# Optimization experiments

Measured on AMD Instinct MI355X. Metric: run time of the kernel, lower is better.

The kernel has to match this reference:

```python
import jax, jax.numpy as jnp
import numpy as np
from functools import partial

H = 512          # hidden_size
H4 = H // 4      # goal hidden size
ENC = 8          # enc_steps
DEC = 12         # dec_steps
PRED = 2         # pred_dim (ETH)
B = 512          # batch


def _lin(k, i, o, s=0.05):
    kw, kb = jax.random.split(k)
    return jax.random.normal(kw, (i, o), jnp.float32) * s, jax.random.normal(kb, (o,), jnp.float32) * s


def setup_inputs() -> dict:
    key = jax.random.key(0)
    ks = jax.random.split(key, 32)
    d = {"inputs": jax.random.normal(ks[0], (B, ENC, 6), jnp.float32)}
    d["embed_w"], d["embed_b"] = _lin(ks[1], 6, H)
    d["reg_w"], d["reg_b"] = _lin(ks[2], H, PRED)
    d["ea_w"], d["ea_b"] = _lin(ks[3], H4, 1)
    d["da_w"], d["da_b"] = _lin(ks[4], H4, 1)
    d["e2g_w"], d["e2g_b"] = _lin(ks[5], H, H4)
    d["e2d_w"], d["e2d_b"] = _lin(ks[6], H, H)
    d["gh2i_w"], d["gh2i_b"] = _lin(ks[7], H4, H4)
    d["dh2i_w"], d["dh2i_b"] = _lin(ks[8], H, H)
    d["gh2t_w"], d["gh2t_b"] = _lin(ks[9], H4, H)
    d["g2e_w"], d["g2e_b"] = _lin(ks[10], H4, H4)
    d["g2d_w"], d["g2d_b"] = _lin(ks[11], H4, H4)
    d["enc_wih"], _ = _lin(ks[12], H + H4, 3 * H)
    d["enc_whh"], _ = _lin(ks[13], H, 3 * H)
    d["enc_bih"] = jax.random.normal(ks[14], (3 * H,), jnp.float32) * 0.05
    d["enc_bhh"] = jax.random.normal(ks[15], (3 * H,), jnp.float32) * 0.05
    d["goal_wih"], _ = _lin(ks[16], H4, 3 * H4)
    d["goal_whh"], _ = _lin(ks[17], H4, 3 * H4)
    d["goal_bih"] = jax.random.normal(ks[18], (3 * H4,), jnp.float32) * 0.05
    d["goal_bhh"] = jax.random.normal(ks[19], (3 * H4,), jnp.float32) * 0.05
    d["dec_wih"], _ = _lin(ks[20], H + H4, 3 * H)
    d["dec_whh"], _ = _lin(ks[21], H, 3 * H)
    d["dec_bih"] = jax.random.normal(ks[22], (3 * H,), jnp.float32) * 0.05
    d["dec_bhh"] = jax.random.normal(ks[23], (3 * H,), jnp.float32) * 0.05
    return d


def _gru(x, h, wih, whh, bih, bhh):
    gi = x @ wih + bih          # [B, 3H]
    gh = h @ whh + bhh
    ir, iz, inn = jnp.split(gi, 3, axis=-1)
    hr, hz, hn = jnp.split(gh, 3, axis=-1)
    r = jax.nn.sigmoid(ir + hr)
    z = jax.nn.sigmoid(iz + hz)
    n = jnp.tanh(inn + r * hn)
    return (1.0 - z) * n + z * h


def reference(inputs, embed_w, embed_b, reg_w, reg_b, ea_w, ea_b, da_w, da_b,
              e2g_w, e2g_b, e2d_w, e2d_b, gh2i_w, gh2i_b, dh2i_w, dh2i_b,
              gh2t_w, gh2t_b, g2e_w, g2e_b, g2d_w, g2d_b,
              enc_wih, enc_whh, enc_bih, enc_bhh,
              goal_wih, goal_whh, goal_bih, goal_bhh,
              dec_wih, dec_whh, dec_bih, dec_bhh):
    relu = jax.nn.relu
    b = inputs.shape[0]
    traj_input = relu(inputs @ embed_w + embed_b)           # [B, ENC, H]

    def sge(goal_hidden):
        def gstep(carry, _):
            gh, gi = carry
            gh = _gru(gi, gh, goal_wih, goal_whh, goal_bih, goal_bhh)
            gi = relu(gh @ gh2i_w + gh2i_b)
            return (gh, gi), gh
        gi0 = jnp.zeros((b, H4), traj_input.dtype)
        _, goals = jax.lax.scan(gstep, (goal_hidden, gi0), None, length=DEC)  # [DEC,B,H4]
        goal_traj = relu(goals @ gh2t_w + gh2t_b) @ reg_w + reg_b             # [DEC,B,PRED]
        goal_for_dec = relu(goals @ g2d_w + g2d_b)                            # [DEC,B,H4]
        gfe = relu(goals @ g2e_w + g2e_b).transpose(1, 0, 2)                  # [B,DEC,H4]
        logits = relu(jnp.tanh(gfe) @ ea_w + ea_b)[..., 0]                    # [B,DEC]
        attn = jax.nn.softmax(logits, axis=1)
        goal_for_enc = jnp.einsum('bt,bth->bh', attn, gfe)
        return goal_for_dec, goal_for_enc, goal_traj.transpose(1, 0, 2)

    def decoder(dec_hidden, gfd):
        gfd_b = gfd.transpose(1, 0, 2)  # [B,DEC,H4]
        steps = jnp.arange(DEC)
        def dstep(dh, t):
            mask = (steps >= t)[None, :, None]
            gdi = jnp.where(mask, gfd_b, 0.0)                      # zeros before t, faithful to torch
            logits = relu(jnp.tanh(gdi) @ da_w + da_b)[..., 0]     # [B,DEC]
            attn = jax.nn.softmax(logits, axis=1)
            ctx = jnp.einsum('bt,bth->bh', attn, gdi)
            ddi = relu(dh @ dh2i_w + dh2i_b)
            x = jnp.concatenate([ctx, ddi], axis=-1)
            dh = _gru(x, dh, dec_wih, dec_whh, dec_bih, dec_bhh)
            return dh, dh @ reg_w + reg_b
        _, traj = jax.lax.scan(dstep, dec_hidden, steps)           # [DEC,B,PRED]
        return traj.transpose(1, 0, 2)

    def estep(carry, x_t):
        teh, gfe = carry
        teh = _gru(jnp.concatenate([x_t, gfe], axis=1), teh,
                   enc_wih, enc_whh, enc_bih, enc_bhh)
        goal_hidden = relu(teh @ e2g_w + e2g_b)
        dec_hidden = relu(teh @ e2d_w + e2d_b)
        gfd, gfe, goal_traj = sge(goal_hidden)
        dec_traj = decoder(dec_hidden, gfd)
        return (teh, gfe), (goal_traj, dec_traj)

    teh0 = jnp.zeros((b, H), traj_input.dtype)
    gfe0 = jnp.zeros((b, H4), traj_input.dtype)
    _, (all_goal, all_dec) = jax.lax.scan(estep, (teh0, gfe0),
                                          traj_input.transpose(1, 0, 2))
    # [ENC,B,DEC,PRED] -> [B,ENC,DEC,PRED]
    return all_goal.transpose(1, 0, 2, 3), all_dec.transpose(1, 0, 2, 3)
```

## Files before the change

kernel.cpp:

```cpp
#include <hip/hip_runtime.h>


typedef unsigned short u16;
typedef __attribute__((ext_vector_type(8))) short bf16x8;
typedef __attribute__((ext_vector_type(4))) float f32x4;

static __device__ __forceinline__ float b2f(u16 u) {
  union { float f; unsigned int i; } x; x.i = ((unsigned int)u) << 16; return x.f;
}
static __device__ __forceinline__ u16 f2b(float f) {
  unsigned int u = __float_as_uint(f);
  unsigned int r = (u + 0x7FFFu + ((u >> 16) & 1u)) >> 16;
  return (u16)r;
}
static __device__ __forceinline__ float fsig(float x) {
  return __fdividef(1.f, 1.f + __expf(-x));
}
static __device__ __forceinline__ float ftanh(float x) {
  return 1.f - __fdividef(2.f, __expf(2.f * x) + 1.f);
}

__global__ __launch_bounds__(256) void transpose_f2b(const float* __restrict__ in,
                                                     u16* __restrict__ out,
                                                     int K, int N) {
  __shared__ u16 t[32][33];
  int n0 = blockIdx.x * 32, k0 = blockIdx.y * 32;
  int x = threadIdx.x & 31, y = threadIdx.x >> 5;
  for (int i = 0; i < 4; i++) t[y + 8 * i][x] = f2b(in[(size_t)(k0 + y + 8 * i) * N + n0 + x]);
  __syncthreads();
  for (int i = 0; i < 4; i++) out[(size_t)(n0 + y + 8 * i) * K + k0 + x] = t[x][y + 8 * i];
}

__global__ __launch_bounds__(256) void embed_kernel(const float* __restrict__ inp,
                                                    const float* __restrict__ w,
                                                    const float* __restrict__ bias,
                                                    u16* __restrict__ traj) {
  int t = blockIdx.x * 256 + threadIdx.x;
  int h = t & 511, b = (t >> 9) & 511, e = t >> 18;
  float acc = bias[h];
  for (int i = 0; i < 6; i++) acc += inp[(b * 8 + e) * 6 + i] * w[i * 512 + h];
  traj[((e * 512) + b) * 512 + h] = f2b(fmaxf(acc, 0.f));
}

__global__ __launch_bounds__(256) void copy_xt(const u16* __restrict__ traj_e,
                                               u16* __restrict__ xcat) {
  int t = blockIdx.x * 256 + threadIdx.x;
  int r = t >> 6, c8 = (t & 63) * 8;
  *(uint4*)&xcat[r * 640 + c8] = *(const uint4*)&traj_e[r * 512 + c8];
}

__global__ __launch_bounds__(256) void gemm_bt(const u16* __restrict__ A, int lda,
                                               const u16* __restrict__ W, int ldw,
                                               const float* __restrict__ bias,
                                               u16* __restrict__ Cb, int ldc,
                                               float* __restrict__ Cf,
                                               int K, int relu) {
  __shared__ u16 As[64][72];
  __shared__ u16 Bs[64][72];
  int tid = threadIdx.x;
  int m0 = blockIdx.y * 64, n0 = blockIdx.x * 64;
  int lane = tid & 63, wave = tid >> 6;
  int wr = wave >> 1, wc = wave & 1;
  int mrow = lane & 15, kq = (lane >> 4) * 8;
  f32x4 acc[2][2] = {};

  for (int k0 = 0; k0 < K; k0 += 64) {
    __syncthreads();
    for (int c = tid; c < 512; c += 256) {
      int r = c >> 3, kk = (c & 7) * 8;
      *(uint4*)&As[r][kk] = *(const uint4*)&A[(size_t)(m0 + r) * lda + k0 + kk];
      *(uint4*)&Bs[r][kk] = *(const uint4*)&W[(size_t)(n0 + r) * ldw + k0 + kk];
    }
    __syncthreads();
    for (int ks = 0; ks < 2; ks++) {
      bf16x8 af[2], bf[2];
      for (int i = 0; i < 2; i++) {
        af[i] = *(const bf16x8*)&As[wr * 32 + i * 16 + mrow][ks * 32 + kq];
        bf[i] = *(const bf16x8*)&Bs[wc * 32 + i * 16 + mrow][ks * 32 + kq];
      }
      for (int i = 0; i < 2; i++)
        for (int j = 0; j < 2; j++)
          acc[i][j] = __builtin_amdgcn_mfma_f32_16x16x32_bf16(af[i], bf[j], acc[i][j], 0, 0, 0);
    }
  }
  int col = lane & 15, rq = (lane >> 4) * 4;
  for (int i = 0; i < 2; i++)
    for (int j = 0; j < 2; j++) {
      int n = n0 + wc * 32 + j * 16 + col;
      float bv = bias ? bias[n] : 0.f;
      for (int r = 0; r < 4; r++) {
        int m = m0 + wr * 32 + i * 16 + rq + r;
        float v = acc[i][j][r] + bv;
        if (relu) v = fmaxf(v, 0.f);
        Cb[(size_t)m * ldc + n] = f2b(v);
        if (Cf) Cf[(size_t)m * ldc + n] = v;
      }
    }
}

struct GDesc {
  const u16* A; int lda;
  const u16* W; int ldw;
  const float* bias;
  u16* Cb; int ldc;
  float* Cf;
  u16* Cb2; int ldc2; int route_n;
  int K; int relu; int nblk;
};

__global__ __launch_bounds__(256) void gemm128(GDesc d0, GDesc d1) {
  GDesc d = (blockIdx.z == 0) ? d0 : d1;
  if ((int)blockIdx.x >= d.nblk) return;
  __shared__ u16 As[128][72];
  __shared__ u16 Bs[128][72];
  int tid = threadIdx.x;
  int m0 = blockIdx.y * 128, n0 = blockIdx.x * 128;
  int lane = tid & 63, wave = tid >> 6;
  int wr = wave >> 1, wc = wave & 1;
  int mrow = lane & 15, kq = (lane >> 4) * 8;
  int srow = tid >> 3, scol = (tid & 7) * 8;
  f32x4 acc[4][4] = {};

  for (int k0 = 0; k0 < d.K; k0 += 64) {
    __syncthreads();
#pragma unroll
    for (int p = 0; p < 4; p++) {
      int r = srow + p * 32;
      *(uint4*)&As[r][scol] = *(const uint4*)&d.A[(size_t)(m0 + r) * d.lda + k0 + scol];
      *(uint4*)&Bs[r][scol] = *(const uint4*)&d.W[(size_t)(n0 + r) * d.ldw + k0 + scol];
    }
    __syncthreads();
#pragma unroll
    for (int ks = 0; ks < 2; ks++) {
      bf16x8 af[4], bf[4];
#pragma unroll
      for (int i = 0; i < 4; i++) {
        af[i] = *(const bf16x8*)&As[wr * 64 + i * 16 + mrow][ks * 32 + kq];
        bf[i] = *(const bf16x8*)&Bs[wc * 64 + i * 16 + mrow][ks * 32 + kq];
      }
#pragma unroll
      for (int i = 0; i < 4; i++)
#pragma unroll
        for (int j = 0; j < 4; j++)
          acc[i][j] = __builtin_amdgcn_mfma_f32_16x16x32_bf16(af[i], bf[j], acc[i][j], 0, 0, 0);
    }
  }
  int col = lane & 15, rq = (lane >> 4) * 4;
#pragma unroll
  for (int j = 0; j < 4; j++) {
    int n = n0 + wc * 64 + j * 16 + col;
    float bv = d.bias ? d.bias[n] : 0.f;
    bool r2 = (n >= d.route_n);
    u16* cb = r2 ? d.Cb2 : d.Cb;
    int ldc = r2 ? d.ldc2 : d.ldc;
    int nn = r2 ? n - d.route_n : n;
#pragma unroll
    for (int i = 0; i < 4; i++)
#pragma unroll
      for (int r = 0; r < 4; r++) {
        int m = m0 + wr * 64 + i * 16 + rq + r;
        float v = acc[i][j][r] + bv;
        if (d.relu) v = fmaxf(v, 0.f);
        cb[(size_t)m * ldc + nn] = f2b(v);
        if (d.Cf) d.Cf[(size_t)m * d.ldc + n] = v;
      }
  }
}

__global__ __launch_bounds__(256) void gru_pw(const u16* __restrict__ gi,
                                              const u16* __restrict__ gh,
                                              float* __restrict__ hf,
                                              u16* __restrict__ hb, int rows) {
  int t = blockIdx.x * 256 + threadIdx.x;
  if (t >= rows * 64) return;
  int r = t >> 6, j8 = (t & 63) * 8;
  size_t base = (size_t)r * 1536 + j8;
  uint4 ir4 = *(const uint4*)&gi[base];
  uint4 iz4 = *(const uint4*)&gi[base + 512];
  uint4 in4 = *(const uint4*)&gi[base + 1024];
  uint4 hr4 = *(const uint4*)&gh[base];
  uint4 hz4 = *(const uint4*)&gh[base + 512];
  uint4 hn4 = *(const uint4*)&gh[base + 1024];
  const u16* irp = (const u16*)&ir4; const u16* izp = (const u16*)&iz4;
  const u16* inp = (const u16*)&in4; const u16* hrp = (const u16*)&hr4;
  const u16* hzp = (const u16*)&hz4; const u16* hnp = (const u16*)&hn4;
  size_t hoff = (size_t)r * 512 + j8;
  float hv[8];
  *(float4*)&hv[0] = *(const float4*)&hf[hoff];
  *(float4*)&hv[4] = *(const float4*)&hf[hoff + 4];
  u16 hbv[8];
  for (int j = 0; j < 8; j++) {
    float rr = fsig(b2f(irp[j]) + b2f(hrp[j]));
    float zz = fsig(b2f(izp[j]) + b2f(hzp[j]));
    float nn = ftanh(b2f(inp[j]) + rr * b2f(hnp[j]));
    float ho = (1.f - zz) * nn + zz * hv[j];
    hv[j] = ho; hbv[j] = f2b(ho);
  }
  *(float4*)&hf[hoff] = *(const float4*)&hv[0];
  *(float4*)&hf[hoff + 4] = *(const float4*)&hv[4];
  *(uint4*)&hb[hoff] = *(const uint4*)&hbv[0];
}

__global__ __launch_bounds__(1024) void goal_mega(const u16* __restrict__ gh0,
                                                  const u16* __restrict__ wih_t,
                                                  const u16* __restrict__ whh_t,
                                                  const float* __restrict__ bih,
                                                  const float* __restrict__ bhh,
                                                  const u16* __restrict__ g2i_t,
                                                  const float* __restrict__ g2i_b,
                                                  const u16* __restrict__ g2e_t,
                                                  const float* __restrict__ g2e_b,
                                                  const float* __restrict__ eaw,
                                                  const float* __restrict__ eab,
                                                  u16* __restrict__ goals,
                                                  u16* __restrict__ xcat) {
  __shared__ float ghf[16][128];
  __shared__ u16   ghb[16][136];
  __shared__ u16   gib[16][136];
  __shared__ float gi3[16][388];
  __shared__ float gh3[16][388];
  __shared__ u16   gfe_l[12][16][128];
  int tid = threadIdx.x;
  int r0 = blockIdx.x * 16;
  int lane = tid & 63, wave = tid >> 6;
  int mrow = lane & 15, kq = (lane >> 4) * 8;
  int rq4 = (lane >> 4) * 4;

  bf16x8 Bf[3][4];
  float  bias1[3];
  int    n0s[3];
  bool   isIv[3];
#pragma unroll
  for (int i = 0; i < 3; i++) {
    int tt = wave + 16 * i;
    bool iI = tt < 24;
    int n0 = (iI ? tt : tt - 24) * 16;
    isIv[i] = iI; n0s[i] = n0;
    const u16* Wt = iI ? wih_t : whh_t;
#pragma unroll
    for (int ks = 0; ks < 4; ks++)
      Bf[i][ks] = *(const bf16x8*)&Wt[(n0 + mrow) * 128 + ks * 32 + kq];
    bias1[i] = (iI ? bih : bhh)[n0 + mrow];
  }
  bf16x8 Gf[4];
  float bias3;
  {
    const u16* W3 = (wave < 8) ? g2i_t : g2e_t;
    const float* B3 = (wave < 8) ? g2i_b : g2e_b;
    int n0 = (wave & 7) * 16;
#pragma unroll
    for (int ks = 0; ks < 4; ks++)
      Gf[ks] = *(const bf16x8*)&W3[(n0 + mrow) * 128 + ks * 32 + kq];
    bias3 = B3[n0 + mrow];
  }

  for (int idx = tid; idx < 16 * 128; idx += 1024) {
    int m = idx >> 7, j = idx & 127;
    u16 u = gh0[(r0 + m) * 128 + j];
    ghb[m][j] = u; ghf[m][j] = b2f(u); gib[m][j] = 0;
  }
  __syncthreads();

  for (int t = 0; t < 12; t++) {
    bf16x8 agi[4], agh[4];
#pragma unroll
    for (int ks = 0; ks < 4; ks++) {
      agi[ks] = *(const bf16x8*)&gib[mrow][ks * 32 + kq];
      agh[ks] = *(const bf16x8*)&ghb[mrow][ks * 32 + kq];
    }
#pragma unroll
    for (int i = 0; i < 3; i++) {
      f32x4 acc = {};
#pragma unroll
      for (int ks = 0; ks < 4; ks++)
        acc = __builtin_amdgcn_mfma_f32_16x16x32_bf16(isIv[i] ? agi[ks] : agh[ks],
                                                      Bf[i][ks], acc, 0, 0, 0);
      float* G = isIv[i] ? &gi3[0][0] : &gh3[0][0];
      int n = n0s[i] + mrow;
#pragma unroll
      for (int r = 0; r < 4; r++)
        G[(rq4 + r) * 388 + n] = acc[r] + bias1[i];
    }
    __syncthreads();
    for (int idx = tid; idx < 2048; idx += 1024) {
      int m = idx >> 7, j = idx & 127;
      float rr = fsig(gi3[m][j] + gh3[m][j]);
      float zz = fsig(gi3[m][128 + j] + gh3[m][128 + j]);
      float nn = ftanh(gi3[m][256 + j] + rr * gh3[m][256 + j]);
      float h = ghf[m][j];
      float ho = (1.f - zz) * nn + zz * h;
      ghf[m][j] = ho;
      u16 hb = f2b(ho);
      ghb[m][j] = hb;
      goals[(t * 512 + r0 + m) * 128 + j] = hb;
    }
    __syncthreads();
    {
      f32x4 acc = {};
#pragma unroll
      for (int ks = 0; ks < 4; ks++) {
        bf16x8 a = *(const bf16x8*)&ghb[mrow][ks * 32 + kq];
        acc = __builtin_amdgcn_mfma_f32_16x16x32_bf16(a, Gf[ks], acc, 0, 0, 0);
      }
      int n = (wave & 7) * 16 + mrow;
      if (wave < 8) {
#pragma unroll
        for (int r = 0; r < 4; r++)
          gib[rq4 + r][n] = f2b(fmaxf(acc[r] + bias3, 0.f));
      } else {
#pragma unroll
        for (int r = 0; r < 4; r++)
          gfe_l[t][rq4 + r][n] = f2b(fmaxf(acc[r] + bias3, 0.f));
      }
    }
    __syncthreads();
  }

  {
    int m = wave;
    float w0 = eaw[lane], w1 = eaw[lane + 64];
    float eb = eab[0];
    float v0[12], v1[12], lg[12];
#pragma unroll
    for (int t = 0; t < 12; t++) {
      float a = b2f(gfe_l[t][m][lane]);
      float c = b2f(gfe_l[t][m][lane + 64]);
      v0[t] = a; v1[t] = c;
      float p = ftanh(a) * w0 + ftanh(c) * w1;
      for (int o = 32; o; o >>= 1) p += __shfl_xor(p, o);
      lg[t] = fmaxf(p + eb, 0.f);
    }
    float mx = lg[0];
#pragma unroll
    for (int t = 1; t < 12; t++) mx = fmaxf(mx, lg[t]);
    float s = 0.f;
#pragma unroll
    for (int t = 0; t < 12; t++) { lg[t] = __expf(lg[t] - mx); s += lg[t]; }
    float inv = __fdividef(1.f, s);
    float c0 = 0.f, c1 = 0.f;
#pragma unroll
    for (int t = 0; t < 12; t++) { c0 += lg[t] * inv * v0[t]; c1 += lg[t] * inv * v1[t]; }
    xcat[(r0 + m) * 640 + 512 + lane] = f2b(c0);
    xcat[(r0 + m) * 640 + 512 + lane + 64] = f2b(c1);
  }
}

__global__ __launch_bounds__(256) void regdot(const u16* __restrict__ X,
                                              const float* __restrict__ rw,
                                              const float* __restrict__ rb,
                                              float* __restrict__ out, int mode, int param) {
  int wid = (blockIdx.x * 256 + threadIdx.x) >> 6;
  int lane = threadIdx.x & 63;
  int row = wid;
  int k0 = lane * 8;
  uint4 xv = *(const uint4*)&X[(size_t)row * 512 + k0];
  const u16* xp = (const u16*)&xv;
  float p0 = 0.f, p1 = 0.f;
  for (int j = 0; j < 8; j++) {
    float x = b2f(xp[j]);
    p0 += x * rw[(k0 + j) * 2];
    p1 += x * rw[(k0 + j) * 2 + 1];
  }
  for (int o = 32; o; o >>= 1) { p0 += __shfl_down(p0, o); p1 += __shfl_down(p1, o); }
  if (lane == 0) {
    int b, e, td;
    if (mode == 1) { td = param; e = row >> 9; b = row & 511; }
    else { int s = row >> 9; e = s / 12; td = s - e * 12; b = row & 511; }
    size_t off = ((size_t)(b * 8 + e) * 12 + td) * 2;
    out[off]     = p0 + rb[0];
    out[off + 1] = p1 + rb[1];
  }
}

__global__ __launch_bounds__(64) void attn_dec_k(const u16* __restrict__ gfd,
                                                 const float* __restrict__ daw,
                                                 const float* __restrict__ dab,
                                                 u16* __restrict__ xdec, int td) {
  int row = blockIdx.x;
  int lane = threadIdx.x;
  int e = row >> 9, b = row & 511;
  int h0 = lane, h1 = lane + 64;
  float w0 = daw[h0], w1 = daw[h1];
  float bias = dab[0];
  float base = fmaxf(bias, 0.f);
  float v0[12], v1[12], lg[12];
  for (int s = 0; s < 12; s++) {
    if (s < td) { lg[s] = base; v0[s] = 0.f; v1[s] = 0.f; }
    else {
      size_t o = ((size_t)(e * 12 + s) * 512 + b) * 128;
      float a = b2f(gfd[o + h0]);
      float c = b2f(gfd[o + h1]);
      v0[s] = a; v1[s] = c;
      float p = ftanh(a) * w0 + ftanh(c) * w1;
      for (int o2 = 32; o2; o2 >>= 1) p += __shfl_xor(p, o2);
      lg[s] = fmaxf(p + bias, 0.f);
    }
  }
  float m = lg[0];
  for (int s = 1; s < 12; s++) m = fmaxf(m, lg[s]);
  float ssum = 0.f;
  for (int s = 0; s < 12; s++) { lg[s] = __expf(lg[s] - m); ssum += lg[s]; }
  float inv = __fdividef(1.f, ssum);
  float c0 = 0.f, c1 = 0.f;
  for (int s = 0; s < 12; s++) { c0 += lg[s] * inv * v0[s]; c1 += lg[s] * inv * v1[s]; }
  xdec[(size_t)row * 640 + h0] = f2b(c0);
  xdec[(size_t)row * 640 + h1] = f2b(c1);
}

extern "C" void kernel_launch(void* const* d_in, const int* in_sizes, int n_in,
                              void* d_out, int out_size, void* d_ws, size_t ws_size,
                              hipStream_t stream) {
  const float* inp      = (const float*)d_in[0];
  const float* embed_w  = (const float*)d_in[1];
  const float* embed_b  = (const float*)d_in[2];
  const float* reg_w    = (const float*)d_in[3];
  const float* reg_b    = (const float*)d_in[4];
  const float* ea_w     = (const float*)d_in[5];
  const float* ea_b     = (const float*)d_in[6];
  const float* da_w     = (const float*)d_in[7];
  const float* da_b     = (const float*)d_in[8];
  const float* e2g_w    = (const float*)d_in[9];
  const float* e2g_b    = (const float*)d_in[10];
  const float* e2d_w    = (const float*)d_in[11];
  const float* e2d_b    = (const float*)d_in[12];
  const float* gh2i_w   = (const float*)d_in[13];
  const float* gh2i_b   = (const float*)d_in[14];
  const float* dh2i_w   = (const float*)d_in[15];
  const float* dh2i_b   = (const float*)d_in[16];
  const float* gh2t_w   = (const float*)d_in[17];
  const float* gh2t_b   = (const float*)d_in[18];
  const float* g2e_w    = (const float*)d_in[19];
  const float* g2e_b    = (const float*)d_in[20];
  const float* g2d_w    = (const float*)d_in[21];
  const float* g2d_b    = (const float*)d_in[22];
  const float* enc_wih  = (const float*)d_in[23];
  const float* enc_whh  = (const float*)d_in[24];
  const float* enc_bih  = (const float*)d_in[25];
  const float* enc_bhh  = (const float*)d_in[26];
  const float* goal_wih = (const float*)d_in[27];
  const float* goal_whh = (const float*)d_in[28];
  const float* goal_bih = (const float*)d_in[29];
  const float* goal_bhh = (const float*)d_in[30];
  const float* dec_wih  = (const float*)d_in[31];
  const float* dec_whh  = (const float*)d_in[32];
  const float* dec_bih  = (const float*)d_in[33];
  const float* dec_bhh  = (const float*)d_in[34];

  char* ws = (char*)d_ws;
  size_t off = 0;
  auto alloc = [&](size_t bytes) -> char* {
    char* p = ws + off; off += (bytes + 255) & ~(size_t)255; return p;
  };
  const size_t TSZ = 512 * 512;
  float* teh_f    = (float*)alloc(TSZ * 4);
  u16*   teh_hist = (u16*)  alloc(9 * TSZ * 2);
  u16*   xcat     = (u16*)  alloc(512 * 640 * 2);
  u16*   traj     = (u16*)  alloc((size_t)8 * TSZ * 2);
  u16*   gh0      = (u16*)  alloc(512 * 128 * 2);
  u16*   goals_all= (u16*)  alloc((size_t)8 * 6144 * 128 * 2);
  u16*   ghid     = (u16*)  alloc((size_t)49152 * 512 * 2);
  u16*   gfd      = (u16*)  alloc((size_t)49152 * 128 * 2);
  float* dh_f     = (float*)alloc((size_t)4096 * 512 * 4);
  u16*   dh_b     = (u16*)  alloc((size_t)4096 * 512 * 2);
  u16*   xdec     = (u16*)  alloc((size_t)4096 * 640 * 2);
  u16*   giD      = (u16*)  alloc((size_t)4096 * 1536 * 2);
  u16*   ghD      = (u16*)  alloc((size_t)4096 * 1536 * 2);
  u16*   giE = giD, *ghE = ghD;
  u16* enc_wih_t  = (u16*)alloc((size_t)1536 * 640 * 2);
  u16* enc_whh_t  = (u16*)alloc((size_t)1536 * 512 * 2);
  u16* dec_wih_t  = (u16*)alloc((size_t)1536 * 640 * 2);
  u16* dec_whh_t  = (u16*)alloc((size_t)1536 * 512 * 2);
  u16* e2g_t      = (u16*)alloc(128 * 512 * 2);
  u16* e2d_t      = (u16*)alloc(512 * 512 * 2);
  u16* dh2i_t     = (u16*)alloc(512 * 512 * 2);
  u16* head_t     = (u16*)alloc(640 * 128 * 2);
  u16* g2e_t      = (u16*)alloc(128 * 128 * 2);
  u16* goal_wih_t = (u16*)alloc(384 * 128 * 2);
  u16* goal_whh_t = (u16*)alloc(384 * 128 * 2);
  u16* gh2i_t     = (u16*)alloc(128 * 128 * 2);
  float* head_b   = (float*)alloc(640 * 4);
  if (off > ws_size) return;

  float* out_goal = (float*)d_out;
  float* out_dec  = out_goal + (size_t)512 * 8 * 12 * 2;

  hipMemsetAsync(teh_f, 0, TSZ * 4 + TSZ * 2, stream);
  hipMemsetAsync(xcat, 0, 512 * 640 * 2, stream);

  auto T = [&](const float* in, u16* out, int K, int N) {
    transpose_f2b<<<dim3(N / 32, K / 32), 256, 0, stream>>>(in, out, K, N);
  };
  T(enc_wih, enc_wih_t, 640, 1536);
  T(enc_whh, enc_whh_t, 512, 1536);
  T(dec_wih, dec_wih_t, 640, 1536);
  T(dec_whh, dec_whh_t, 512, 1536);
  T(e2g_w, e2g_t, 512, 128);
  T(e2d_w, e2d_t, 512, 512);
  T(dh2i_w, dh2i_t, 512, 512);
  T(gh2t_w, head_t, 128, 512);
  T(g2d_w, head_t + 512 * 128, 128, 128);
  T(g2e_w, g2e_t, 128, 128);
  T(goal_wih, goal_wih_t, 128, 384);
  T(goal_whh, goal_whh_t, 128, 384);
  T(gh2i_w, gh2i_t, 128, 128);
  hipMemcpyAsync(head_b, gh2t_b, 512 * 4, hipMemcpyDeviceToDevice, stream);
  hipMemcpyAsync(head_b + 512, g2d_b, 128 * 4, hipMemcpyDeviceToDevice, stream);

  embed_kernel<<<8192, 256, 0, stream>>>(inp, embed_w, embed_b, traj);

  const int FAR = 1 << 30;
  auto G64 = [&](const u16* A, int lda, const u16* W, int ldw, const float* bias,
                 u16* Cb, int ldc, float* Cf, int M, int N, int K, int relu) {
    gemm_bt<<<dim3(N / 64, M / 64), 256, 0, stream>>>(A, lda, W, ldw, bias, Cb, ldc, Cf, K, relu);
  };

  for (int e = 0; e < 8; ++e) {
    copy_xt<<<128, 256, 0, stream>>>(traj + (size_t)e * TSZ, xcat);
    GDesc dgi{xcat, 640, enc_wih_t, 640, enc_bih, giE, 1536, nullptr,
              nullptr, 0, FAR, 640, 0, 12};
    GDesc dgh{teh_hist + e * TSZ, 512, enc_whh_t, 512, enc_bhh, ghE, 1536, nullptr,
              nullptr, 0, FAR, 512, 0, 12};
    gemm128<<<dim3(12, 4, 2), 256, 0, stream>>>(dgi, dgh);
    gru_pw<<<128, 256, 0, stream>>>(giE, ghE, teh_f, teh_hist + (e + 1) * TSZ, 512);
    G64(teh_hist + (e + 1) * TSZ, 512, e2g_t, 512, e2g_b, gh0, 128, nullptr, 512, 128, 512, 1);
    goal_mega<<<32, 1024, 0, stream>>>(gh0, goal_wih_t, goal_whh_t, goal_bih, goal_bhh,
                                       gh2i_t, gh2i_b, g2e_t, g2e_b, ea_w, ea_b,
                                       goals_all + (size_t)e * 6144 * 128, xcat);
  }

  {
    GDesc de2d{teh_hist + TSZ, 512, e2d_t, 512, e2d_b, dh_b, 512, dh_f,
               nullptr, 0, FAR, 512, 1, 4};
    gemm128<<<dim3(4, 32, 1), 256, 0, stream>>>(de2d, de2d);
    GDesc dhead{goals_all, 128, head_t, 128, head_b, ghid, 512, nullptr,
                gfd, 128, 512, 128, 1, 5};
    gemm128<<<dim3(5, 384, 1), 256, 0, stream>>>(dhead, dhead);
    regdot<<<12288, 256, 0, stream>>>(ghid, reg_w, reg_b, out_goal, 2, 0);
  }

  for (int td = 0; td < 12; ++td) {
    attn_dec_k<<<4096, 64, 0, stream>>>(gfd, da_w, da_b, xdec, td);
    GDesc dd1{dh_b, 512, dh2i_t, 512, dh2i_b, xdec + 128, 640, nullptr,
              nullptr, 0, FAR, 512, 1, 4};
    GDesc dd2{dh_b, 512, dec_whh_t, 512, dec_bhh, ghD, 1536, nullptr,
              nullptr, 0, FAR, 512, 0, 12};
    gemm128<<<dim3(12, 32, 2), 256, 0, stream>>>(dd1, dd2);
    GDesc dgi{xdec, 640, dec_wih_t, 640, dec_bih, giD, 1536, nullptr,
              nullptr, 0, FAR, 640, 0, 12};
    gemm128<<<dim3(12, 32, 1), 256, 0, stream>>>(dgi, dgi);
    gru_pw<<<1024, 256, 0, stream>>>(giD, ghD, dh_f, dh_b, 4096);
    regdot<<<1024, 256, 0, stream>>>(dh_b, reg_w, reg_b, out_dec, 1, td);
  }
}
```

Before: 1.524 ms.

## Fuse GRU pointwise, e2g and regression into neighbors; batch transposes and attention

Merges the 13 weight transposes into one launch. The gemm can now read its A operand from two sources, which removes the xcat copy and the concat buffers. The encoder GRU pointwise step and the e2g projection move into goal_mega, and the decoder regression head is folded into the GRU pointwise kernel. Decoder attention for all 12 steps is precomputed in a single kernel before the loop. These changes aim to cut kernel launches and intermediate global round-trips, at the cost of more shared memory in goal_mega and a larger xctx buffer.

```diff
diff --git a/kernel.cpp b/kernel.cpp
--- a/kernel.cpp
+++ b/kernel.cpp
@@ -20,15 +20,28 @@
   return 1.f - __fdividef(2.f, __expf(2.f * x) + 1.f);
 }
 
-__global__ __launch_bounds__(256) void transpose_f2b(const float* __restrict__ in,
-                                                     u16* __restrict__ out,
-                                                     int K, int N) {
-  __shared__ u16 t[32][33];
-  int n0 = blockIdx.x * 32, k0 = blockIdx.y * 32;
+struct TransArgs {
+  const float* in[13];
+  u16* out[13];
+  int K[13], N[13], t0[13], nx[13];
+};
+
+__global__ __launch_bounds__(256) void transpose_all(TransArgs ta) {
+  int bid = blockIdx.x;
+  int i = 0;
+  for (int k = 1; k < 13; k++) if (bid >= ta.t0[k]) i = k;
+  const float* in = ta.in[i];
+  u16* out = ta.out[i];
+  int K = ta.K[i], N = ta.N[i];
+  int local = bid - ta.t0[i];
+  int nx = ta.nx[i];
+  int tx = local % nx, ty = local / nx;
+  __shared__ u16 tbuf[32][33];
+  int n0 = tx * 32, k0 = ty * 32;
   int x = threadIdx.x & 31, y = threadIdx.x >> 5;
-  for (int i = 0; i < 4; i++) t[y + 8 * i][x] = f2b(in[(size_t)(k0 + y + 8 * i) * N + n0 + x]);
+  for (int q = 0; q < 4; q++) tbuf[y + 8 * q][x] = f2b(in[(size_t)(k0 + y + 8 * q) * N + n0 + x]);
   __syncthreads();
-  for (int i = 0; i < 4; i++) out[(size_t)(n0 + y + 8 * i) * K + k0 + x] = t[x][y + 8 * i];
+  for (int q = 0; q < 4; q++) out[(size_t)(n0 + y + 8 * q) * K + k0 + x] = tbuf[x][y + 8 * q];
 }
 
 __global__ __launch_bounds__(256) void embed_kernel(const float* __restrict__ inp,
@@ -42,64 +55,9 @@
   traj[((e * 512) + b) * 512 + h] = f2b(fmaxf(acc, 0.f));
 }
 
-__global__ __launch_bounds__(256) void copy_xt(const u16* __restrict__ traj_e,
-                                               u16* __restrict__ xcat) {
-  int t = blockIdx.x * 256 + threadIdx.x;
-  int r = t >> 6, c8 = (t & 63) * 8;
-  *(uint4*)&xcat[r * 640 + c8] = *(const uint4*)&traj_e[r * 512 + c8];
-}
-
-__global__ __launch_bounds__(256) void gemm_bt(const u16* __restrict__ A, int lda,
-                                               const u16* __restrict__ W, int ldw,
-                                               const float* __restrict__ bias,
-                                               u16* __restrict__ Cb, int ldc,
-                                               float* __restrict__ Cf,
-                                               int K, int relu) {
-  __shared__ u16 As[64][72];
-  __shared__ u16 Bs[64][72];
-  int tid = threadIdx.x;
-  int m0 = blockIdx.y * 64, n0 = blockIdx.x * 64;
-  int lane = tid & 63, wave = tid >> 6;
-  int wr = wave >> 1, wc = wave & 1;
-  int mrow = lane & 15, kq = (lane >> 4) * 8;
-  f32x4 acc[2][2] = {};
-
-  for (int k0 = 0; k0 < K; k0 += 64) {
-    __syncthreads();
-    for (int c = tid; c < 512; c += 256) {
-      int r = c >> 3, kk = (c & 7) * 8;
-      *(uint4*)&As[r][kk] = *(const uint4*)&A[(size_t)(m0 + r) * lda + k0 + kk];
-      *(uint4*)&Bs[r][kk] = *(const uint4*)&W[(size_t)(n0 + r) * ldw + k0 + kk];
-    }
-    __syncthreads();
-    for (int ks = 0; ks < 2; ks++) {
-      bf16x8 af[2], bf[2];
-      for (int i = 0; i < 2; i++) {
-        af[i] = *(const bf16x8*)&As[wr * 32 + i * 16 + mrow][ks * 32 + kq];
-        bf[i] = *(const bf16x8*)&Bs[wc * 32 + i * 16 + mrow][ks * 32 + kq];
-      }
-      for (int i = 0; i < 2; i++)
-        for (int j = 0; j < 2; j++)
-          acc[i][j] = __builtin_amdgcn_mfma_f32_16x16x32_bf16(af[i], bf[j], acc[i][j], 0, 0, 0);
-    }
-  }
-  int col = lane & 15, rq = (lane >> 4) * 4;
-  for (int i = 0; i < 2; i++)
-    for (int j = 0; j < 2; j++) {
-      int n = n0 + wc * 32 + j * 16 + col;
-      float bv = bias ? bias[n] : 0.f;
-      for (int r = 0; r < 4; r++) {
-        int m = m0 + wr * 32 + i * 16 + rq + r;
-        float v = acc[i][j][r] + bv;
-        if (relu) v = fmaxf(v, 0.f);
-        Cb[(size_t)m * ldc + n] = f2b(v);
-        if (Cf) Cf[(size_t)m * ldc + n] = v;
-      }
-    }
-}
-
 struct GDesc {
   const u16* A; int lda;
+  const u16* A2; int lda2; int asplit;
   const u16* W; int ldw;
   const float* bias;
   u16* Cb; int ldc;
@@ -122,11 +80,14 @@
   f32x4 acc[4][4] = {};
 
   for (int k0 = 0; k0 < d.K; k0 += 64) {
+    const u16* Asrc; int Alda, kk;
+    if (k0 < d.asplit) { Asrc = d.A; Alda = d.lda; kk = k0; }
+    else               { Asrc = d.A2; Alda = d.lda2; kk = k0 - d.asplit; }
     __syncthreads();
 #pragma unroll
     for (int p = 0; p < 4; p++) {
       int r = srow + p * 32;
-      *(uint4*)&As[r][scol] = *(const uint4*)&d.A[(size_t)(m0 + r) * d.lda + k0 + scol];
+      *(uint4*)&As[r][scol] = *(const uint4*)&Asrc[(size_t)(m0 + r) * Alda + kk + scol];
       *(uint4*)&Bs[r][scol] = *(const uint4*)&d.W[(size_t)(n0 + r) * d.ldw + k0 + scol];
     }
     __syncthreads();
@@ -167,13 +128,16 @@
   }
 }
 
-__global__ __launch_bounds__(256) void gru_pw(const u16* __restrict__ gi,
-                                              const u16* __restrict__ gh,
-                                              float* __restrict__ hf,
-                                              u16* __restrict__ hb, int rows) {
+__global__ __launch_bounds__(256) void gru_pw_reg(const u16* __restrict__ gi,
+                                                  const u16* __restrict__ gh,
+                                                  float* __restrict__ hf,
+                                                  u16* __restrict__ hb,
+                                                  const float* __restrict__ rw,
+                                                  const float* __restrict__ rb,
+                                                  float* __restrict__ out, int td) {
   int t = blockIdx.x * 256 + threadIdx.x;
-  if (t >= rows * 64) return;
-  int r = t >> 6, j8 = (t & 63) * 8;
+  int r = t >> 6, lane = threadIdx.x & 63;
+  int j8 = lane * 8;
   size_t base = (size_t)r * 1536 + j8;
   uint4 ir4 = *(const uint4*)&gi[base];
   uint4 iz4 = *(const uint4*)&gi[base + 512];
@@ -189,19 +153,34 @@
   *(float4*)&hv[0] = *(const float4*)&hf[hoff];
   *(float4*)&hv[4] = *(const float4*)&hf[hoff + 4];
   u16 hbv[8];
+  float p0 = 0.f, p1 = 0.f;
   for (int j = 0; j < 8; j++) {
     float rr = fsig(b2f(irp[j]) + b2f(hrp[j]));
     float zz = fsig(b2f(izp[j]) + b2f(hzp[j]));
     float nn = ftanh(b2f(inp[j]) + rr * b2f(hnp[j]));
     float ho = (1.f - zz) * nn + zz * hv[j];
     hv[j] = ho; hbv[j] = f2b(ho);
+    p0 += ho * rw[(j8 + j) * 2];
+    p1 += ho * rw[(j8 + j) * 2 + 1];
   }
   *(float4*)&hf[hoff] = *(const float4*)&hv[0];
   *(float4*)&hf[hoff + 4] = *(const float4*)&hv[4];
   *(uint4*)&hb[hoff] = *(const uint4*)&hbv[0];
-}
-
-__global__ __launch_bounds__(1024) void goal_mega(const u16* __restrict__ gh0,
+  for (int o = 32; o; o >>= 1) { p0 += __shfl_down(p0, o); p1 += __shfl_down(p1, o); }
+  if (lane == 0) {
+    int e = r >> 9, b = r & 511;
+    size_t off = ((size_t)(b * 8 + e) * 12 + td) * 2;
+    out[off] = p0 + rb[0];
+    out[off + 1] = p1 + rb[1];
+  }
+}
+
+__global__ __launch_bounds__(1024) void goal_mega(const u16* __restrict__ gi_g,
+                                                  const u16* __restrict__ gh_g,
+                                                  float* __restrict__ teh_f,
+                                                  u16* __restrict__ teh_out,
+                                                  const u16* __restrict__ e2g_t,
+                                                  const float* __restrict__ e2g_b,
                                                   const u16* __restrict__ wih_t,
                                                   const u16* __restrict__ whh_t,
                                                   const float* __restrict__ bih,
@@ -213,13 +192,14 @@
                                                   const float* __restrict__ eaw,
                                                   const float* __restrict__ eab,
                                                   u16* __restrict__ goals,
-                                                  u16* __restrict__ xcat) {
+                                                  u16* __restrict__ gfe_out) {
   __shared__ float ghf[16][128];
   __shared__ u16   ghb[16][136];
   __shared__ u16   gib[16][136];
   __shared__ float gi3[16][388];
   __shared__ float gh3[16][388];
   __shared__ u16   gfe_l[12][16][128];
+  __shared__ u16   tehb[16][520];
   int tid = threadIdx.x;
   int r0 = blockIdx.x * 16;
   int lane = tid & 63, wave = tid >> 6;
@@ -254,10 +234,62 @@
     bias3 = B3[n0 + mrow];
   }
 
-  for (int idx = tid; idx < 16 * 128; idx += 1024) {
-    int m = idx >> 7, j = idx & 127;
-    u16 u = gh0[(r0 + m) * 128 + j];
-    ghb[m][j] = u; ghf[m][j] = b2f(u); gib[m][j] = 0;
+  {
+    u16* gz = &gib[0][0];
+    for (int idx = tid; idx < 16 * 136; idx += 1024) gz[idx] = 0;
+  }
+
+  {
+    int r = wave;
+    int j8 = lane * 8;
+    int grow = r0 + r;
+    size_t base = (size_t)grow * 1536 + j8;
+    uint4 ir4 = *(const uint4*)&gi_g[base];
+    uint4 iz4 = *(const uint4*)&gi_g[base + 512];
+    uint4 in4 = *(const uint4*)&gi_g[base + 1024];
+    uint4 hr4 = *(const uint4*)&gh_g[base];
+    uint4 hz4 = *(const uint4*)&gh_g[base + 512];
+    uint4 hn4 = *(const uint4*)&gh_g[base + 1024];
+    const u16* irp = (const u16*)&ir4; const u16* izp = (const u16*)&iz4;
+    const u16* inp = (const u16*)&in4; const u16* hrp = (const u16*)&hr4;
+    const u16* hzp = (const u16*)&hz4; const u16* hnp = (const u16*)&hn4;
+    size_t hoff = (size_t)grow * 512 + j8;
+    float hv[8];
+    *(float4*)&hv[0] = *(const float4*)&teh_f[hoff];
+    *(float4*)&hv[4] = *(const float4*)&teh_f[hoff + 4];
+    u16 hbv[8];
+    for (int j = 0; j < 8; j++) {
+      float rr = fsig(b2f(irp[j]) + b2f(hrp[j]));
+      float zz = fsig(b2f(izp[j]) + b2f(hzp[j]));
+      float nn = ftanh(b2f(inp[j]) + rr * b2f(hnp[j]));
+      float ho = (1.f - zz) * nn + zz * hv[j];
+      hv[j] = ho; hbv[j] = f2b(ho);
+    }
+    *(float4*)&teh_f[hoff] = *(const float4*)&hv[0];
+    *(float4*)&teh_f[hoff + 4] = *(const float4*)&hv[4];
+    *(uint4*)&teh_out[hoff] = *(const uint4*)&hbv[0];
+    *(uint4*)&tehb[r][j8] = *(const uint4*)&hbv[0];
+  }
+  __syncthreads();
+
+  if (wave < 8) {
+    int n0 = wave * 16;
+    f32x4 acc = {};
+#pragma unroll
+    for (int ks = 0; ks < 16; ks++) {
+      bf16x8 a = *(const bf16x8*)&tehb[mrow][ks * 32 + kq];
+      bf16x8 b = *(const bf16x8*)&e2g_t[(size_t)(n0 + mrow) * 512 + ks * 32 + kq];
+      acc = __builtin_amdgcn_mfma_f32_16x16x32_bf16(a, b, acc, 0, 0, 0);
+    }
+    int n = n0 + mrow;
+    float bv = e2g_b[n];
+#pragma unroll
+    for (int r = 0; r < 4; r++) {
+      float v = fmaxf(acc[r] + bv, 0.f);
+      int m = rq4 + r;
+      ghf[m][n] = v;
+      ghb[m][n] = f2b(v);
+    }
   }
   __syncthreads();
 
@@ -340,18 +372,17 @@
     float c0 = 0.f, c1 = 0.f;
 #pragma unroll
     for (int t = 0; t < 12; t++) { c0 += lg[t] * inv * v0[t]; c1 += lg[t] * inv * v1[t]; }
-    xcat[(r0 + m) * 640 + 512 + lane] = f2b(c0);
-    xcat[(r0 + m) * 640 + 512 + lane + 64] = f2b(c1);
-  }
-}
-
-__global__ __launch_bounds__(256) void regdot(const u16* __restrict__ X,
-                                              const float* __restrict__ rw,
-                                              const float* __restrict__ rb,
-                                              float* __restrict__ out, int mode, int param) {
-  int wid = (blockIdx.x * 256 + threadIdx.x) >> 6;
+    gfe_out[(r0 + m) * 128 + lane] = f2b(c0);
+    gfe_out[(r0 + m) * 128 + lane + 64] = f2b(c1);
+  }
+}
+
+__global__ __launch_bounds__(256) void regdot_goal(const u16* __restrict__ X,
+                                                   const float* __restrict__ rw,
+                                                   const float* __restrict__ rb,
+                                                   float* __restrict__ out) {
+  int row = (blockIdx.x * 256 + threadIdx.x) >> 6;
   int lane = threadIdx.x & 63;
-  int row = wid;
   int k0 = lane * 8;
   uint4 xv = *(const uint4*)&X[(size_t)row * 512 + k0];
   const u16* xp = (const u16*)&xv;
@@ -363,48 +394,56 @@
   }
   for (int o = 32; o; o >>= 1) { p0 += __shfl_down(p0, o); p1 += __shfl_down(p1, o); }
   if (lane == 0) {
-    int b, e, td;
-    if (mode == 1) { td = param; e = row >> 9; b = row & 511; }
-    else { int s = row >> 9; e = s / 12; td = s - e * 12; b = row & 511; }
+    int s = row >> 9, b = row & 511;
+    int e = s / 12, td = s - e * 12;
     size_t off = ((size_t)(b * 8 + e) * 12 + td) * 2;
-    out[off]     = p0 + rb[0];
+    out[off] = p0 + rb[0];
     out[off + 1] = p1 + rb[1];
   }
 }
 
-__global__ __launch_bounds__(64) void attn_dec_k(const u16* __restrict__ gfd,
-                                                 const float* __restrict__ daw,
-                                                 const float* __restrict__ dab,
-                                                 u16* __restrict__ xdec, int td) {
+__global__ __launch_bounds__(256) void attn_ctx_all(const u16* __restrict__ gfd,
+                                                    const float* __restrict__ daw,
+                                                    const float* __restrict__ dab,
+                                                    u16* __restrict__ xctx) {
+  __shared__ u16 rowbuf[1536];
   int row = blockIdx.x;
-  int lane = threadIdx.x;
+  int tid = threadIdx.x;
   int e = row >> 9, b = row & 511;
-  int h0 = lane, h1 = lane + 64;
-  float w0 = daw[h0], w1 = daw[h1];
+  for (int idx = tid; idx < 1536; idx += 256) {
+    int s = idx >> 7, h = idx & 127;
+    rowbuf[idx] = gfd[((size_t)(e * 12 + s) * 512 + b) * 128 + h];
+  }
+  __syncthreads();
+  int lane = tid & 63, wave = tid >> 6;
+  float w0 = daw[lane], w1 = daw[lane + 64];
   float bias = dab[0];
   float base = fmaxf(bias, 0.f);
-  float v0[12], v1[12], lg[12];
-  for (int s = 0; s < 12; s++) {
-    if (s < td) { lg[s] = base; v0[s] = 0.f; v1[s] = 0.f; }
-    else {
-      size_t o = ((size_t)(e * 12 + s) * 512 + b) * 128;
-      float a = b2f(gfd[o + h0]);
-      float c = b2f(gfd[o + h1]);
-      v0[s] = a; v1[s] = c;
-      float p = ftanh(a) * w0 + ftanh(c) * w1;
-      for (int o2 = 32; o2; o2 >>= 1) p += __shfl_xor(p, o2);
-      lg[s] = fmaxf(p + bias, 0.f);
-    }
-  }
-  float m = lg[0];
-  for (int s = 1; s < 12; s++) m = fmaxf(m, lg[s]);
-  float ssum = 0.f;
-  for (int s = 0; s < 12; s++) { lg[s] = __expf(lg[s] - m); ssum += lg[s]; }
-  float inv = __fdividef(1.f, ssum);
-  float c0 = 0.f, c1 = 0.f;
-  for (int s = 0; s < 12; s++) { c0 += lg[s] * inv * v0[s]; c1 += lg[s] * inv * v1[s]; }
-  xdec[(size_t)row * 640 + h0] = f2b(c0);
-  xdec[(size_t)row * 640 + h1] = f2b(c1);
+  for (int q = 0; q < 3; q++) {
+    int td = wave + q * 4;
+    float v0[12], v1[12], lg[12];
+    for (int s = 0; s < 12; s++) {
+      if (s < td) { lg[s] = base; v0[s] = 0.f; v1[s] = 0.f; }
+      else {
+        float a = b2f(rowbuf[s * 128 + lane]);
+        float c = b2f(rowbuf[s * 128 + 64 + lane]);
+        v0[s] = a; v1[s] = c;
+        float p = ftanh(a) * w0 + ftanh(c) * w1;
+        for (int o = 32; o; o >>= 1) p += __shfl_xor(p, o);
+        lg[s] = fmaxf(p + bias, 0.f);
+      }
+    }
+    float m = lg[0];
+    for (int s = 1; s < 12; s++) m = fmaxf(m, lg[s]);
+    float ssum = 0.f;
+    for (int s = 0; s < 12; s++) { lg[s] = __expf(lg[s] - m); ssum += lg[s]; }
+    float inv = __fdividef(1.f, ssum);
+    float c0 = 0.f, c1 = 0.f;
+    for (int s = 0; s < 12; s++) { c0 += lg[s] * inv * v0[s]; c1 += lg[s] * inv * v1[s]; }
+    size_t o = ((size_t)td * 4096 + row) * 128;
+    xctx[o + lane] = f2b(c0);
+    xctx[o + lane + 64] = f2b(c1);
+  }
 }
 
 extern "C" void kernel_launch(void* const* d_in, const int* in_sizes, int n_in,
@@ -454,15 +493,16 @@
   const size_t TSZ = 512 * 512;
   float* teh_f    = (float*)alloc(TSZ * 4);
   u16*   teh_hist = (u16*)  alloc(9 * TSZ * 2);
-  u16*   xcat     = (u16*)  alloc(512 * 640 * 2);
+  u16*   gfe_buf  = (u16*)  alloc(512 * 128 * 2);
+  size_t zero_bytes = off;
   u16*   traj     = (u16*)  alloc((size_t)8 * TSZ * 2);
-  u16*   gh0      = (u16*)  alloc(512 * 128 * 2);
   u16*   goals_all= (u16*)  alloc((size_t)8 * 6144 * 128 * 2);
   u16*   ghid     = (u16*)  alloc((size_t)49152 * 512 * 2);
   u16*   gfd      = (u16*)  alloc((size_t)49152 * 128 * 2);
+  u16*   xctx     = (u16*)  alloc((size_t)12 * 4096 * 128 * 2);
   float* dh_f     = (float*)alloc((size_t)4096 * 512 * 4);
   u16*   dh_b     = (u16*)  alloc((size_t)4096 * 512 * 2);
-  u16*   xdec     = (u16*)  alloc((size_t)4096 * 640 * 2);
+  u16*   ddi      = (u16*)  alloc((size_t)4096 * 512 * 2);
   u16*   giD      = (u16*)  alloc((size_t)4096 * 1536 * 2);
   u16*   ghD      = (u16*)  alloc((size_t)4096 * 1536 * 2);
   u16*   giE = giD, *ghE = ghD;
@@ -484,71 +524,76 @@
   float* out_goal = (float*)d_out;
   float* out_dec  = out_goal + (size_t)512 * 8 * 12 * 2;
 
-  hipMemsetAsync(teh_f, 0, TSZ * 4 + TSZ * 2, stream);
-  hipMemsetAsync(xcat, 0, 512 * 640 * 2, stream);
-
-  auto T = [&](const float* in, u16* out, int K, int N) {
-    transpose_f2b<<<dim3(N / 32, K / 32), 256, 0, stream>>>(in, out, K, N);
+  hipMemsetAsync(teh_f, 0, zero_bytes, stream);
+
+  TransArgs ta;
+  int ntile = 0, ti = 0;
+  auto push = [&](const float* in, u16* out, int K, int N) {
+    ta.in[ti] = in; ta.out[ti] = out; ta.K[ti] = K; ta.N[ti] = N;
+    ta.t0[ti] = ntile; ta.nx[ti] = N / 32;
+    ntile += (K / 32) * (N / 32); ti++;
   };
-  T(enc_wih, enc_wih_t, 640, 1536);
-  T(enc_whh, enc_whh_t, 512, 1536);
-  T(dec_wih, dec_wih_t, 640, 1536);
-  T(dec_whh, dec_whh_t, 512, 1536);
-  T(e2g_w, e2g_t, 512, 128);
-  T(e2d_w, e2d_t, 512, 512);
-  T(dh2i_w, dh2i_t, 512, 512);
-  T(gh2t_w, head_t, 128, 512);
-  T(g2d_w, head_t + 512 * 128, 128, 128);
-  T(g2e_w, g2e_t, 128, 128);
-  T(goal_wih, goal_wih_t, 128, 384);
-  T(goal_whh, goal_whh_t, 128, 384);
-  T(gh2i_w, gh2i_t, 128, 128);
+  push(enc_wih, enc_wih_t, 640, 1536);
+  push(enc_whh, enc_whh_t, 512, 1536);
+  push(dec_wih, dec_wih_t, 640, 1536);
+  push(dec_whh, dec_whh_t, 512, 1536);
+  push(e2g_w, e2g_t, 512, 128);
+  push(e2d_w, e2d_t, 512, 512);
+  push(dh2i_w, dh2i_t, 512, 512);
+  push(gh2t_w, head_t, 128, 512);
+  push(g2d_w, head_t + 512 * 128, 128, 128);
+  push(g2e_w, g2e_t, 128, 128);
+  push(goal_wih, goal_wih_t, 128, 384);
+  push(goal_whh, goal_whh_t, 128, 384);
+  push(gh2i_w, gh2i_t, 128, 128);
+  transpose_all<<<ntile, 256, 0, stream>>>(ta);
   hipMemcpyAsync(head_b, gh2t_b, 512 * 4, hipMemcpyDeviceToDevice, stream);
   hipMemcpyAsync(head_b + 512, g2d_b, 128 * 4, hipMemcpyDeviceToDevice, stream);
 
   embed_kernel<<<8192, 256, 0, stream>>>(inp, embed_w, embed_b, traj);
 
   const int FAR = 1 << 30;
-  auto G64 = [&](const u16* A, int lda, const u16* W, int ldw, const float* bias,
-                 u16* Cb, int ldc, float* Cf, int M, int N, int K, int relu) {
-    gemm_bt<<<dim3(N / 64, M / 64), 256, 0, stream>>>(A, lda, W, ldw, bias, Cb, ldc, Cf, K, relu);
-  };
 
   for (int e = 0; e < 8; ++e) {
-    copy_xt<<<128, 256, 0, stream>>>(traj + (size_t)e * TSZ, xcat);
-    GDesc dgi{xcat, 640, enc_wih_t, 640, enc_bih, giE, 1536, nullptr,
+    GDesc dgi{traj + (size_t)e * TSZ, 512, gfe_buf, 128, 512,
+              enc_wih_t, 640, enc_bih, giE, 1536, nullptr,
               nullptr, 0, FAR, 640, 0, 12};
-    GDesc dgh{teh_hist + e * TSZ, 512, enc_whh_t, 512, enc_bhh, ghE, 1536, nullptr,
+    GDesc dgh{teh_hist + (size_t)e * TSZ, 512, nullptr, 0, FAR,
+              enc_whh_t, 512, enc_bhh, ghE, 1536, nullptr,
               nullptr, 0, FAR, 512, 0, 12};
     gemm128<<<dim3(12, 4, 2), 256, 0, stream>>>(dgi, dgh);
-    gru_pw<<<128, 256, 0, stream>>>(giE, ghE, teh_f, teh_hist + (e + 1) * TSZ, 512);
-    G64(teh_hist + (e + 1) * TSZ, 512, e2g_t, 512, e2g_b, gh0, 128, nullptr, 512, 128, 512, 1);
-    goal_mega<<<32, 1024, 0, stream>>>(gh0, goal_wih_t, goal_whh_t, goal_bih, goal_bhh,
+    goal_mega<<<32, 1024, 0, stream>>>(giE, ghE, teh_f, teh_hist + (size_t)(e + 1) * TSZ,
+                                       e2g_t, e2g_b,
+                                       goal_wih_t, goal_whh_t, goal_bih, goal_bhh,
                                        gh2i_t, gh2i_b, g2e_t, g2e_b, ea_w, ea_b,
-                                       goals_all + (size_t)e * 6144 * 128, xcat);
+                                       goals_all + (size_t)e * 6144 * 128, gfe_buf);
   }
 
   {
-    GDesc de2d{teh_hist + TSZ, 512, e2d_t, 512, e2d_b, dh_b, 512, dh_f,
+    GDesc de2d{teh_hist + TSZ, 512, nullptr, 0, FAR,
+               e2d_t, 512, e2d_b, dh_b, 512, dh_f,
                nullptr, 0, FAR, 512, 1, 4};
     gemm128<<<dim3(4, 32, 1), 256, 0, stream>>>(de2d, de2d);
-    GDesc dhead{goals_all, 128, head_t, 128, head_b, ghid, 512, nullptr,
+    GDesc dhead{goals_all, 128, nullptr, 0, FAR,
+                head_t, 128, head_b, ghid, 512, nullptr,
                 gfd, 128, 512, 128, 1, 5};
     gemm128<<<dim3(5, 384, 1), 256, 0, stream>>>(dhead, dhead);
-    regdot<<<12288, 256, 0, stream>>>(ghid, reg_w, reg_b, out_goal, 2, 0);
+    regdot_goal<<<12288, 256, 0, stream>>>(ghid, reg_w, reg_b, out_goal);
+    attn_ctx_all<<<4096, 256, 0, stream>>>(gfd, da_w, da_b, xctx);
   }
 
   for (int td = 0; td < 12; ++td) {
-    attn_dec_k<<<4096, 64, 0, stream>>>(gfd, da_w, da_b, xdec, td);
-    GDesc dd1{dh_b, 512, dh2i_t, 512, dh2i_b, xdec + 128, 640, nullptr,
+    GDesc dd1{dh_b, 512, nullptr, 0, FAR,
+              dh2i_t, 512, dh2i_b, ddi, 512, nullptr,
               nullptr, 0, FAR, 512, 1, 4};
-    GDesc dd2{dh_b, 512, dec_whh_t, 512, dec_bhh, ghD, 1536, nullptr,
+    GDesc dd2{dh_b, 512, nullptr, 0, FAR,
+              dec_whh_t, 512, dec_bhh, ghD, 1536, nullptr,
               nullptr, 0, FAR, 512, 0, 12};
     gemm128<<<dim3(12, 32, 2), 256, 0, stream>>>(dd1, dd2);
-    GDesc dgi{xdec, 640, dec_wih_t, 640, dec_bih, giD, 1536, nullptr,
+    GDesc dgi{xctx + (size_t)td * 4096 * 128, 128, ddi, 512, 128,
+              dec_wih_t, 640, dec_bih, giD, 1536, nullptr,
               nullptr, 0, FAR, 640, 0, 12};
     gemm128<<<dim3(12, 32, 1), 256, 0, stream>>>(dgi, dgi);
-    gru_pw<<<1024, 256, 0, stream>>>(giD, ghD, dh_f, dh_b, 4096);
-    regdot<<<1024, 256, 0, stream>>>(dh_b, reg_w, reg_b, out_dec, 1, td);
-  }
-}
+    gru_pw_reg<<<1024, 256, 0, stream>>>(giD, ghD, dh_f, dh_b, reg_w, reg_b, out_dec, td);
+  }
+}
```

Measured after the change: 1.356 ms. -11.0%, faster.
